# Kernel optimization log

Hardware: AMD Instinct MI355X
Metric: run time of the kernel (lower is better)

The kernel has to match this reference:

```python
import jax, jax.numpy as jnp
import numpy as np

FIVE = 6            # top-k features kept per output unit
OUT, IN, HID, B = 512, 1024, 32, 256


def setup_inputs() -> dict:
    key = jax.random.key(0)
    ks = jax.random.split(key, 6)
    return {
        "inputs": jax.random.normal(ks[0], (B, IN), jnp.float32),
        "mask": jax.random.normal(ks[1], (OUT, IN), jnp.float32),
        "W1": jax.random.normal(ks[2], (OUT, IN, HID), jnp.float32) / 2.236,
        "W2": jax.random.normal(ks[3], (OUT, HID, HID), jnp.float32) / HID ** 0.5,
        "W3": jax.random.normal(ks[4], (OUT, HID, HID), jnp.float32) / HID ** 0.5,
        "W4": jax.random.normal(ks[5], (OUT, HID, 1), jnp.float32) / HID ** 0.5,
    }


def reference(inputs, mask, W1, W2, W3, W4):
    # top-k binary mask: 1 at the FIVE largest entries of each row of mask
    _, idx = jax.lax.top_k(mask, FIVE)                       # (out, FIVE)
    rows = jnp.arange(mask.shape[0])[:, None]
    m = jnp.zeros_like(mask).at[rows, idx].set(1.0)          # (out, in)

    # gated inputs, broadcast of torch's bmm outer-product trick:
    # x[o,b,i] = inputs[b,i] * m[o,i]
    x = inputs[None, :, :] * m[:, None, :]                   # (out, batch, in)

    # per-output-unit 4-layer MLP (batched over 'o')
    h = jax.nn.relu(jnp.einsum('obi,oih->obh', x, W1))       # (out, batch, hid)
    h = jax.nn.relu(jnp.einsum('obh,ohk->obk', h, W2))
    h = jax.nn.relu(jnp.einsum('obh,ohk->obk', h, W3))
    y = jnp.einsum('obh,oh->ob', h, W4[:, :, 0])             # (out, batch)
    y = jax.nn.sigmoid(y).T                                  # (batch, out)

    # STE binarize (forward value)
    q = (y >= 0.5).astype(y.dtype) * 2.0 - 1.0
    return q
```

## Files before the change

### kernel.cpp

```cpp
#include <hip/hip_runtime.h>
#include <math.h>

#define NOUT 512
#define NIN  1024
#define HID  32
#define NB   256
#define TOPK 6

__global__ __launch_bounds__(256, 2) void blayer_kernel(
    const float* __restrict__ inputs,
    const float* __restrict__ mask,
    const float* __restrict__ W1,
    const float* __restrict__ W2,
    const float* __restrict__ W3,
    const float* __restrict__ W4,
    float* __restrict__ out)
{
    const int o = blockIdx.x;
    const int t = threadIdx.x;

    __shared__ float vals[NIN];
    __shared__ int   sidx[TOPK];
    __shared__ float red_v[4];
    __shared__ int   red_i[4];

    const float* mrow = mask + (size_t)o * NIN;
#pragma unroll
    for (int k = 0; k < NIN / NB; ++k) vals[t + NB * k] = mrow[t + NB * k];
    __syncthreads();

    for (int it = 0; it < TOPK; ++it) {
        float bv = -INFINITY;
        int   bi = 0;
#pragma unroll
        for (int k = 0; k < NIN / NB; ++k) {
            float v = vals[t + NB * k];
            if (v > bv) { bv = v; bi = t + NB * k; }
        }
#pragma unroll
        for (int off = 32; off > 0; off >>= 1) {
            float ov = __shfl_down(bv, off);
            int   oi = __shfl_down(bi, off);
            if (ov > bv) { bv = ov; bi = oi; }
        }
        if ((t & 63) == 0) { red_v[t >> 6] = bv; red_i[t >> 6] = bi; }
        __syncthreads();
        if (t == 0) {
            float fv = red_v[0]; int fi = red_i[0];
            for (int w = 1; w < 4; ++w)
                if (red_v[w] > fv) { fv = red_v[w]; fi = red_i[w]; }
            sidx[it] = fi;
            vals[fi] = -INFINITY;
        }
        __syncthreads();
    }

    int sj[TOPK];
#pragma unroll
    for (int j = 0; j < TOPK; ++j)
        sj[j] = __builtin_amdgcn_readfirstlane(sidx[j]);

    float xin[TOPK];
#pragma unroll
    for (int j = 0; j < TOPK; ++j)
        xin[j] = inputs[(size_t)t * NIN + sj[j]];

    const float* W1b = W1 + (size_t)o * NIN * HID;
    const float* W2b = W2 + (size_t)o * HID * HID;
    const float* W3b = W3 + (size_t)o * HID * HID;
    const float* W4b = W4 + (size_t)o * HID;

    float h[HID], acc[HID];

#pragma unroll
    for (int k = 0; k < HID; ++k) acc[k] = 0.0f;
#pragma unroll
    for (int j = 0; j < TOPK; ++j) {
        const float* w1r = W1b + (size_t)sj[j] * HID;
        const float  xj  = xin[j];
#pragma unroll
        for (int k = 0; k < HID; ++k) acc[k] = fmaf(xj, w1r[k], acc[k]);
    }
#pragma unroll
    for (int k = 0; k < HID; ++k) h[k] = acc[k] > 0.0f ? acc[k] : 0.0f;

#pragma unroll
    for (int k = 0; k < HID; ++k) acc[k] = 0.0f;
#pragma unroll
    for (int hh = 0; hh < HID; ++hh) {
        const float hv = h[hh];
        const float* wr = W2b + hh * HID;
#pragma unroll
        for (int k = 0; k < HID; ++k) acc[k] = fmaf(hv, wr[k], acc[k]);
    }
#pragma unroll
    for (int k = 0; k < HID; ++k) h[k] = acc[k] > 0.0f ? acc[k] : 0.0f;

#pragma unroll
    for (int k = 0; k < HID; ++k) acc[k] = 0.0f;
#pragma unroll
    for (int hh = 0; hh < HID; ++hh) {
        const float hv = h[hh];
        const float* wr = W3b + hh * HID;
#pragma unroll
        for (int k = 0; k < HID; ++k) acc[k] = fmaf(hv, wr[k], acc[k]);
    }
#pragma unroll
    for (int k = 0; k < HID; ++k) h[k] = acc[k] > 0.0f ? acc[k] : 0.0f;

    double z = 0.0;
#pragma unroll
    for (int k = 0; k < HID; ++k) z = fma((double)h[k], (double)W4b[k], z);

    out[(size_t)t * NOUT + o] = (z >= 0.0) ? 1.0f : -1.0f;
}

extern "C" void kernel_launch(void* const* d_in, const int* in_sizes, int n_in,
                              void* d_out, int out_size, void* d_ws, size_t ws_size,
                              hipStream_t stream) {
    const float* inputs = (const float*)d_in[0];
    const float* mask   = (const float*)d_in[1];
    const float* W1     = (const float*)d_in[2];
    const float* W2     = (const float*)d_in[3];
    const float* W3     = (const float*)d_in[4];
    const float* W4     = (const float*)d_in[5];
    float* out = (float*)d_out;

    blayer_kernel<<<dim3(NOUT), dim3(NB), 0, stream>>>(
        inputs, mask, W1, W2, W3, W4, out);
}
```

Before: 127.2 us.

## Stage per-unit weights in LDS and compute two batch rows per thread

Each block now uses 128 threads, and each thread evaluates the MLP for two batch rows, so every weight loaded is reused across two rows. The selected W1 rows, W2, W3 and W4 are staged into shared memory as float4 and read from there, replacing per-thread global scalar loads. W2/W3/W4 are prefetched before the top-k selection so the loads overlap it. The cost is roughly double the accumulator registers and fewer threads for the top-k scan.

After: 121.2 us. -4.8%, faster.

```diff
diff --git a/kernel.cpp b/kernel.cpp
--- a/kernel.cpp
+++ b/kernel.cpp
@@ -4,10 +4,11 @@
 #define NOUT 512
 #define NIN  1024
 #define HID  32
-#define NB   256
+#define BATCH 256
+#define NT   128
 #define TOPK 6
 
-__global__ __launch_bounds__(256, 2) void blayer_kernel(
+__global__ __launch_bounds__(NT, 1) void blayer_kernel(
     const float* __restrict__ inputs,
     const float* __restrict__ mask,
     const float* __restrict__ W1,
@@ -19,23 +20,37 @@
     const int o = blockIdx.x;
     const int t = threadIdx.x;
 
-    __shared__ float vals[NIN];
-    __shared__ int   sidx[TOPK];
-    __shared__ float red_v[4];
-    __shared__ int   red_i[4];
+    __shared__ float  vals[NIN];
+    __shared__ int    sidx[TOPK];
+    __shared__ float  red_v[NT / 64];
+    __shared__ int    red_i[NT / 64];
+    __shared__ float4 w1s[TOPK * 8];
+    __shared__ float4 w2s[256];
+    __shared__ float4 w3s[256];
+    __shared__ float4 w4s[8];
+
+    {
+        const float4* W2f = (const float4*)(W2 + (size_t)o * HID * HID);
+        const float4* W3f = (const float4*)(W3 + (size_t)o * HID * HID);
+        w2s[t]       = W2f[t];
+        w2s[t + NT]  = W2f[t + NT];
+        w3s[t]       = W3f[t];
+        w3s[t + NT]  = W3f[t + NT];
+        if (t < 8) w4s[t] = ((const float4*)(W4 + (size_t)o * HID))[t];
+    }
 
     const float* mrow = mask + (size_t)o * NIN;
 #pragma unroll
-    for (int k = 0; k < NIN / NB; ++k) vals[t + NB * k] = mrow[t + NB * k];
+    for (int k = 0; k < NIN / NT; ++k) vals[t + NT * k] = mrow[t + NT * k];
     __syncthreads();
 
     for (int it = 0; it < TOPK; ++it) {
         float bv = -INFINITY;
         int   bi = 0;
 #pragma unroll
-        for (int k = 0; k < NIN / NB; ++k) {
-            float v = vals[t + NB * k];
-            if (v > bv) { bv = v; bi = t + NB * k; }
+        for (int k = 0; k < NIN / NT; ++k) {
+            float v = vals[t + NT * k];
+            if (v > bv) { bv = v; bi = t + NT * k; }
         }
 #pragma unroll
         for (int off = 32; off > 0; off >>= 1) {
@@ -47,8 +62,7 @@
         __syncthreads();
         if (t == 0) {
             float fv = red_v[0]; int fi = red_i[0];
-            for (int w = 1; w < 4; ++w)
-                if (red_v[w] > fv) { fv = red_v[w]; fi = red_i[w]; }
+            if (red_v[1] > fv) { fv = red_v[1]; fi = red_i[1]; }
             sidx[it] = fi;
             vals[fi] = -INFINITY;
         }
@@ -60,59 +74,113 @@
     for (int j = 0; j < TOPK; ++j)
         sj[j] = __builtin_amdgcn_readfirstlane(sidx[j]);
 
-    float xin[TOPK];
+    if (t < TOPK * 8) {
+        int j = t >> 3, q = t & 7;
+        const float4* r = (const float4*)(W1 + ((size_t)o * NIN + sj[j]) * HID);
+        w1s[t] = r[q];
+    }
+
+    float x0[TOPK], x1[TOPK];
 #pragma unroll
-    for (int j = 0; j < TOPK; ++j)
-        xin[j] = inputs[(size_t)t * NIN + sj[j]];
+    for (int j = 0; j < TOPK; ++j) {
+        x0[j] = inputs[(size_t)t * NIN + sj[j]];
+        x1[j] = inputs[(size_t)(t + NT) * NIN + sj[j]];
+    }
+    __syncthreads();
 
-    const float* W1b = W1 + (size_t)o * NIN * HID;
-    const float* W2b = W2 + (size_t)o * HID * HID;
-    const float* W3b = W3 + (size_t)o * HID * HID;
-    const float* W4b = W4 + (size_t)o * HID;
-
-    float h[HID], acc[HID];
+    float a0[HID], a1[HID], c0[HID], c1[HID];
 
 #pragma unroll
-    for (int k = 0; k < HID; ++k) acc[k] = 0.0f;
+    for (int k = 0; k < HID; ++k) { a0[k] = 0.0f; a1[k] = 0.0f; }
 #pragma unroll
     for (int j = 0; j < TOPK; ++j) {
-        const float* w1r = W1b + (size_t)sj[j] * HID;
-        const float  xj  = xin[j];
+        const float v0 = x0[j], v1 = x1[j];
 #pragma unroll
-        for (int k = 0; k < HID; ++k) acc[k] = fmaf(xj, w1r[k], acc[k]);
+        for (int q = 0; q < 8; ++q) {
+            float4 w = w1s[j * 8 + q];
+            a0[4*q+0] = fmaf(v0, w.x, a0[4*q+0]);
+            a0[4*q+1] = fmaf(v0, w.y, a0[4*q+1]);
+            a0[4*q+2] = fmaf(v0, w.z, a0[4*q+2]);
+            a0[4*q+3] = fmaf(v0, w.w, a0[4*q+3]);
+            a1[4*q+0] = fmaf(v1, w.x, a1[4*q+0]);
+            a1[4*q+1] = fmaf(v1, w.y, a1[4*q+1]);
+            a1[4*q+2] = fmaf(v1, w.z, a1[4*q+2]);
+            a1[4*q+3] = fmaf(v1, w.w, a1[4*q+3]);
+        }
     }
 #pragma unroll
-    for (int k = 0; k < HID; ++k) h[k] = acc[k] > 0.0f ? acc[k] : 0.0f;
+    for (int k = 0; k < HID; ++k) {
+        a0[k] = a0[k] > 0.0f ? a0[k] : 0.0f;
+        a1[k] = a1[k] > 0.0f ? a1[k] : 0.0f;
+    }
 
 #pragma unroll
-    for (int k = 0; k < HID; ++k) acc[k] = 0.0f;
+    for (int k = 0; k < HID; ++k) { c0[k] = 0.0f; c1[k] = 0.0f; }
 #pragma unroll
     for (int hh = 0; hh < HID; ++hh) {
-        const float hv = h[hh];
-        const float* wr = W2b + hh * HID;
+        const float v0 = a0[hh], v1 = a1[hh];
 #pragma unroll
-        for (int k = 0; k < HID; ++k) acc[k] = fmaf(hv, wr[k], acc[k]);
+        for (int q = 0; q < 8; ++q) {
+            float4 w = w2s[hh * 8 + q];
+            c0[4*q+0] = fmaf(v0, w.x, c0[4*q+0]);
+            c0[4*q+1] = fmaf(v0, w.y, c0[4*q+1]);
+            c0[4*q+2] = fmaf(v0, w.z, c0[4*q+2]);
+            c0[4*q+3] = fmaf(v0, w.w, c0[4*q+3]);
+            c1[4*q+0] = fmaf(v1, w.x, c1[4*q+0]);
+            c1[4*q+1] = fmaf(v1, w.y, c1[4*q+1]);
+            c1[4*q+2] = fmaf(v1, w.z, c1[4*q+2]);
+            c1[4*q+3] = fmaf(v1, w.w, c1[4*q+3]);
+        }
     }
 #pragma unroll
-    for (int k = 0; k < HID; ++k) h[k] = acc[k] > 0.0f ? acc[k] : 0.0f;
+    for (int k = 0; k < HID; ++k) {
+        c0[k] = c0[k] > 0.0f ? c0[k] : 0.0f;
+        c1[k] = c1[k] > 0.0f ? c1[k] : 0.0f;
+    }
 
 #pragma unroll
-    for (int k = 0; k < HID; ++k) acc[k] = 0.0f;
+    for (int k = 0; k < HID; ++k) { a0[k] = 0.0f; a1[k] = 0.0f; }
 #pragma unroll
     for (int hh = 0; hh < HID; ++hh) {
-        const float hv = h[hh];
-        const float* wr = W3b + hh * HID;
+        const float v0 = c0[hh], v1 = c1[hh];
 #pragma unroll
-        for (int k = 0; k < HID; ++k) acc[k] = fmaf(hv, wr[k], acc[k]);
+        for (int q = 0; q < 8; ++q) {
+            float4 w = w3s[hh * 8 + q];
+            a0[4*q+0] = fmaf(v0, w.x, a0[4*q+0]);
+            a0[4*q+1] = fmaf(v0, w.y, a0[4*q+1]);
+            a0[4*q+2] = fmaf(v0, w.z, a0[4*q+2]);
+            a0[4*q+3] = fmaf(v0, w.w, a0[4*q+3]);
+            a1[4*q+0] = fmaf(v1, w.x, a1[4*q+0]);
+            a1[4*q+1] = fmaf(v1, w.y, a1[4*q+1]);
+            a1[4*q+2] = fmaf(v1, w.z, a1[4*q+2]);
+            a1[4*q+3] = fmaf(v1, w.w, a1[4*q+3]);
+        }
     }
+
+    double z0 = 0.0, z1 = 0.0;
 #pragma unroll
-    for (int k = 0; k < HID; ++k) h[k] = acc[k] > 0.0f ? acc[k] : 0.0f;
+    for (int q = 0; q < 8; ++q) {
+        float4 w = w4s[q];
+        float r00 = a0[4*q+0] > 0.0f ? a0[4*q+0] : 0.0f;
+        float r01 = a0[4*q+1] > 0.0f ? a0[4*q+1] : 0.0f;
+        float r02 = a0[4*q+2] > 0.0f ? a0[4*q+2] : 0.0f;
+        float r03 = a0[4*q+3] > 0.0f ? a0[4*q+3] : 0.0f;
+        float r10 = a1[4*q+0] > 0.0f ? a1[4*q+0] : 0.0f;
+        float r11 = a1[4*q+1] > 0.0f ? a1[4*q+1] : 0.0f;
+        float r12 = a1[4*q+2] > 0.0f ? a1[4*q+2] : 0.0f;
+        float r13 = a1[4*q+3] > 0.0f ? a1[4*q+3] : 0.0f;
+        z0 = fma((double)r00, (double)w.x, z0);
+        z0 = fma((double)r01, (double)w.y, z0);
+        z0 = fma((double)r02, (double)w.z, z0);
+        z0 = fma((double)r03, (double)w.w, z0);
+        z1 = fma((double)r10, (double)w.x, z1);
+        z1 = fma((double)r11, (double)w.y, z1);
+        z1 = fma((double)r12, (double)w.z, z1);
+        z1 = fma((double)r13, (double)w.w, z1);
+    }
 
-    double z = 0.0;
-#pragma unroll
-    for (int k = 0; k < HID; ++k) z = fma((double)h[k], (double)W4b[k], z);
-
-    out[(size_t)t * NOUT + o] = (z >= 0.0) ? 1.0f : -1.0f;
+    out[(size_t)t * NOUT + o]        = (z0 >= 0.0) ? 1.0f : -1.0f;
+    out[(size_t)(t + NT) * NOUT + o] = (z1 >= 0.0) ? 1.0f : -1.0f;
 }
 
 extern "C" void kernel_launch(void* const* d_in, const int* in_sizes, int n_in,
@@ -126,6 +194,6 @@
     const float* W4     = (const float*)d_in[5];
     float* out = (float*)d_out;
 
-    blayer_kernel<<<dim3(NOUT), dim3(NB), 0, stream>>>(
+    blayer_kernel<<<dim3(NOUT), dim3(NT), 0, stream>>>(
         inputs, mask, W1, W2, W3, W4, out);
 }
```

## Run per-unit MLP layers on MFMA with split fp16 hi/lo operands

Applied to the files above, without the earlier changes.

Replaces the per-thread scalar FMA MLP with MFMA 16x16x32 f16 matrix ops. Each fp32 operand is split into a high and a low fp16 part, and four MFMAs per tile recover near-fp32 accuracy. Weights and activations are staged transposed in padded shared memory, with W1's gathered top-k rows packed as the first layer's weight. The goal is to cut the heavy scalar FMA and register cost of the 32x32 layers, in exchange for extra LDS traffic and a small risk of sign flips near zero compared with the earlier double-precision final dot product.

Result: faster. 112.3 us (-11.7%).

```diff
diff --git a/kernel.cpp b/kernel.cpp
--- a/kernel.cpp
+++ b/kernel.cpp
@@ -6,6 +6,71 @@
 #define HID  32
 #define NB   256
 #define TOPK 6
+#define HSTR 40
+
+typedef _Float16 f16x8 __attribute__((ext_vector_type(8)));
+typedef float    f32x4 __attribute__((ext_vector_type(4)));
+
+union HU  { _Float16 h; unsigned short u; };
+union H4U { _Float16 h[4]; unsigned long long u; };
+union H8U { _Float16 h[8]; uint4 u; };
+
+__device__ __forceinline__ unsigned short f16bits(float v) {
+    HU c; c.h = (_Float16)v; return c.u;
+}
+
+template<int NMT>
+__device__ __forceinline__ void mfma_layer(
+    const unsigned short* WtHi, const unsigned short* WtLo,
+    const unsigned short* HHi,  const unsigned short* HLo,
+    int lane15, int quad, int wb, f32x4 acc[NMT][4])
+{
+    f16x8 aH[NMT], aL[NMT], bH[4], bL[4];
+#pragma unroll
+    for (int mt = 0; mt < NMT; ++mt) {
+        int off = (mt * 16 + lane15) * HSTR + quad * 8;
+        aH[mt] = *(const f16x8*)&WtHi[off];
+        aL[mt] = *(const f16x8*)&WtLo[off];
+    }
+#pragma unroll
+    for (int nt = 0; nt < 4; ++nt) {
+        int off = (wb + nt * 16 + lane15) * HSTR + quad * 8;
+        bH[nt] = *(const f16x8*)&HHi[off];
+        bL[nt] = *(const f16x8*)&HLo[off];
+    }
+#pragma unroll
+    for (int mt = 0; mt < NMT; ++mt)
+#pragma unroll
+        for (int nt = 0; nt < 4; ++nt) {
+            acc[mt][nt] = __builtin_amdgcn_mfma_f32_16x16x32_f16(aH[mt], bH[nt], acc[mt][nt], 0, 0, 0);
+            acc[mt][nt] = __builtin_amdgcn_mfma_f32_16x16x32_f16(aH[mt], bL[nt], acc[mt][nt], 0, 0, 0);
+            acc[mt][nt] = __builtin_amdgcn_mfma_f32_16x16x32_f16(aL[mt], bH[nt], acc[mt][nt], 0, 0, 0);
+            acc[mt][nt] = __builtin_amdgcn_mfma_f32_16x16x32_f16(aL[mt], bL[nt], acc[mt][nt], 0, 0, 0);
+        }
+}
+
+__device__ __forceinline__ void store_h(
+    unsigned short* HHi, unsigned short* HLo,
+    int lane15, int quad, int wb, f32x4 acc[2][4])
+{
+#pragma unroll
+    for (int mt = 0; mt < 2; ++mt)
+#pragma unroll
+        for (int nt = 0; nt < 4; ++nt) {
+            H4U hi, lo;
+#pragma unroll
+            for (int r = 0; r < 4; ++r) {
+                float v = acc[mt][nt][r];
+                v = v > 0.0f ? v : 0.0f;
+                _Float16 h = (_Float16)v;
+                hi.h[r] = h;
+                lo.h[r] = (_Float16)(v - (float)h);
+            }
+            int off = (wb + nt * 16 + lane15) * HSTR + mt * 16 + quad * 4;
+            *(unsigned long long*)&HHi[off] = hi.u;
+            *(unsigned long long*)&HLo[off] = lo.u;
+        }
+}
 
 __global__ __launch_bounds__(256, 2) void blayer_kernel(
     const float* __restrict__ inputs,
@@ -18,11 +83,43 @@
 {
     const int o = blockIdx.x;
     const int t = threadIdx.x;
-
+    const int l = t & 63, lane15 = l & 15, quad = l >> 4;
+    const int wb = (t >> 6) * 64;
+
+    __shared__ __align__(16) unsigned short HtHi[NB * HSTR];
+    __shared__ __align__(16) unsigned short HtLo[NB * HSTR];
+    __shared__ __align__(16) unsigned short WHi[3][HID * HSTR];
+    __shared__ __align__(16) unsigned short WLo[3][HID * HSTR];
+    __shared__ __align__(16) unsigned short W4Hi[16 * HSTR];
+    __shared__ __align__(16) unsigned short W4Lo[16 * HSTR];
     __shared__ float vals[NIN];
     __shared__ int   sidx[TOPK];
     __shared__ float red_v[4];
     __shared__ int   red_i[4];
+
+    const float* W2g = W2 + (size_t)o * HID * HID;
+    const float* W3g = W3 + (size_t)o * HID * HID;
+    const float* W4g = W4 + (size_t)o * HID;
+    const float* W1g = W1 + (size_t)o * NIN * HID;
+
+#pragma unroll
+    for (int i = 0; i < 4; ++i) {
+        int e = t + i * 256, m = e & 31, k = e >> 5;
+        float v2 = W2g[e], v3 = W3g[e];
+        _Float16 h2 = (_Float16)v2, h3 = (_Float16)v3;
+        WHi[1][m * HSTR + k] = f16bits(v2);
+        WLo[1][m * HSTR + k] = f16bits(v2 - (float)h2);
+        WHi[2][m * HSTR + k] = f16bits(v3);
+        WLo[2][m * HSTR + k] = f16bits(v3 - (float)h3);
+    }
+#pragma unroll
+    for (int i = 0; i < 2; ++i) {
+        int e = t + i * 256, m = e >> 5, k = e & 31;
+        float v = (m == 0) ? W4g[k] : 0.0f;
+        _Float16 h = (_Float16)v;
+        W4Hi[m * HSTR + k] = f16bits(v);
+        W4Lo[m * HSTR + k] = f16bits(v - (float)h);
+    }
 
     const float* mrow = mask + (size_t)o * NIN;
 #pragma unroll
@@ -55,64 +152,65 @@
         __syncthreads();
     }
 
-    int sj[TOPK];
-#pragma unroll
-    for (int j = 0; j < TOPK; ++j)
-        sj[j] = __builtin_amdgcn_readfirstlane(sidx[j]);
-
-    float xin[TOPK];
-#pragma unroll
-    for (int j = 0; j < TOPK; ++j)
-        xin[j] = inputs[(size_t)t * NIN + sj[j]];
-
-    const float* W1b = W1 + (size_t)o * NIN * HID;
-    const float* W2b = W2 + (size_t)o * HID * HID;
-    const float* W3b = W3 + (size_t)o * HID * HID;
-    const float* W4b = W4 + (size_t)o * HID;
-
-    float h[HID], acc[HID];
-
-#pragma unroll
-    for (int k = 0; k < HID; ++k) acc[k] = 0.0f;
-#pragma unroll
-    for (int j = 0; j < TOPK; ++j) {
-        const float* w1r = W1b + (size_t)sj[j] * HID;
-        const float  xj  = xin[j];
-#pragma unroll
-        for (int k = 0; k < HID; ++k) acc[k] = fmaf(xj, w1r[k], acc[k]);
-    }
-#pragma unroll
-    for (int k = 0; k < HID; ++k) h[k] = acc[k] > 0.0f ? acc[k] : 0.0f;
-
-#pragma unroll
-    for (int k = 0; k < HID; ++k) acc[k] = 0.0f;
-#pragma unroll
-    for (int hh = 0; hh < HID; ++hh) {
-        const float hv = h[hh];
-        const float* wr = W2b + hh * HID;
-#pragma unroll
-        for (int k = 0; k < HID; ++k) acc[k] = fmaf(hv, wr[k], acc[k]);
-    }
-#pragma unroll
-    for (int k = 0; k < HID; ++k) h[k] = acc[k] > 0.0f ? acc[k] : 0.0f;
-
-#pragma unroll
-    for (int k = 0; k < HID; ++k) acc[k] = 0.0f;
-#pragma unroll
-    for (int hh = 0; hh < HID; ++hh) {
-        const float hv = h[hh];
-        const float* wr = W3b + hh * HID;
-#pragma unroll
-        for (int k = 0; k < HID; ++k) acc[k] = fmaf(hv, wr[k], acc[k]);
-    }
-#pragma unroll
-    for (int k = 0; k < HID; ++k) h[k] = acc[k] > 0.0f ? acc[k] : 0.0f;
-
-    double z = 0.0;
-#pragma unroll
-    for (int k = 0; k < HID; ++k) z = fma((double)h[k], (double)W4b[k], z);
-
-    out[(size_t)t * NOUT + o] = (z >= 0.0) ? 1.0f : -1.0f;
+#pragma unroll
+    for (int i = 0; i < 4; ++i) {
+        int e = t + i * 256, m = e & 31, k = e >> 5;
+        float v = (k < TOPK) ? W1g[(size_t)sidx[k] * HID + m] : 0.0f;
+        _Float16 h = (_Float16)v;
+        WHi[0][m * HSTR + k] = f16bits(v);
+        WLo[0][m * HSTR + k] = f16bits(v - (float)h);
+    }
+
+    {
+        int sj[TOPK];
+#pragma unroll
+        for (int j = 0; j < TOPK; ++j)
+            sj[j] = __builtin_amdgcn_readfirstlane(sidx[j]);
+        H8U xh, xl;
+#pragma unroll
+        for (int j = 0; j < 8; ++j) { xh.h[j] = (_Float16)0.0f; xl.h[j] = (_Float16)0.0f; }
+#pragma unroll
+        for (int j = 0; j < TOPK; ++j) {
+            float v = inputs[(size_t)t * NIN + sj[j]];
+            _Float16 h = (_Float16)v;
+            xh.h[j] = h;
+            xl.h[j] = (_Float16)(v - (float)h);
+        }
+        *(uint4*)&HtHi[t * HSTR]      = xh.u;
+        *(uint4*)&HtLo[t * HSTR]      = xl.u;
+        uint4 z = make_uint4(0, 0, 0, 0);
+        *(uint4*)&HtHi[t * HSTR + 8]  = z;
+        *(uint4*)&HtHi[t * HSTR + 16] = z;
+        *(uint4*)&HtHi[t * HSTR + 24] = z;
+        *(uint4*)&HtLo[t * HSTR + 8]  = z;
+        *(uint4*)&HtLo[t * HSTR + 16] = z;
+        *(uint4*)&HtLo[t * HSTR + 24] = z;
+    }
+    __syncthreads();
+
+    f32x4 acc[2][4];
+#pragma unroll
+    for (int L = 0; L < 3; ++L) {
+#pragma unroll
+        for (int mt = 0; mt < 2; ++mt)
+#pragma unroll
+            for (int nt = 0; nt < 4; ++nt) acc[mt][nt] = (f32x4){0.f, 0.f, 0.f, 0.f};
+        mfma_layer<2>(&WHi[L][0], &WLo[L][0], HtHi, HtLo, lane15, quad, wb, acc);
+        store_h(HtHi, HtLo, lane15, quad, wb, acc);
+    }
+
+    f32x4 acc4[1][4];
+#pragma unroll
+    for (int nt = 0; nt < 4; ++nt) acc4[0][nt] = (f32x4){0.f, 0.f, 0.f, 0.f};
+    mfma_layer<1>(W4Hi, W4Lo, HtHi, HtLo, lane15, quad, wb, acc4);
+
+    if (quad == 0) {
+#pragma unroll
+        for (int nt = 0; nt < 4; ++nt) {
+            int b = wb + nt * 16 + lane15;
+            out[(size_t)b * NOUT + o] = (acc4[0][nt][0] >= 0.0f) ? 1.0f : -1.0f;
+        }
+    }
 }
 
 extern "C" void kernel_launch(void* const* d_in, const int* in_sizes, int n_in,
```
